# Optimization experiments

Hardware: AMD Instinct MI355X
Metric: run time of the kernel (lower is better)

The kernel has to match this reference:

```python
import jax, jax.numpy as jnp
import numpy as np

EPS = 1e-5

def layer_norm(x, g, b):
    mu = jnp.mean(x, axis=-1, keepdims=True)
    var = jnp.var(x, axis=-1, keepdims=True)
    return (x - mu) * jax.lax.rsqrt(var + EPS) * g + b

def mlp2_ln(x, w1, b1, g, bt, w2, b2):
    # 2-layer NN: Linear -> LayerNorm -> GELU -> Linear
    h = jax.nn.gelu(layer_norm(x @ w1 + b1, g, bt))
    return h @ w2 + b2

def mlp2(x, w1, b1, w2, b2):
    # 2-layer NN without norm: Linear -> GELU -> Linear
    return jax.nn.gelu(x @ w1 + b1) @ w2 + b2

def setup_inputs() -> dict:
    key = jax.random.key(0)
    ks = jax.random.split(key, 20)
    BS, N, D, M, SG = 64, 10000, 128, 16, 1000
    s = lambda i, shp: jax.random.normal(ks[i], shp, dtype=jnp.float32) * (1.0 / np.sqrt(shp[0]))
    return {
        "node_emb": jax.random.normal(ks[0], (BS, N, D), dtype=jnp.float32),
        "graph_emb": jax.random.normal(ks[1], (BS, D), dtype=jnp.float32),
        "sg_node_idx": jax.random.randint(ks[2], (BS, SG), 0, N),
        "sg_meta_features": jax.random.normal(ks[3], (BS, M), dtype=jnp.float32),
        # sg_net: in 2*D -> D -> D
        "sg_w1": s(4, (2 * D, D)), "sg_b1": jnp.zeros((D,), jnp.float32),
        "sg_g": jnp.ones((D,), jnp.float32), "sg_bt": jnp.zeros((D,), jnp.float32),
        "sg_w2": s(5, (D, D)), "sg_b2": jnp.zeros((D,), jnp.float32),
        # meta_feat_net: M -> D -> D
        "mf_w1": s(6, (M, D)), "mf_b1": jnp.zeros((D,), jnp.float32),
        "mf_g": jnp.ones((D,), jnp.float32), "mf_bt": jnp.zeros((D,), jnp.float32),
        "mf_w2": s(7, (D, D)), "mf_b2": jnp.zeros((D,), jnp.float32),
        # ctxt_net: 2*D -> D -> D, no norm
        "cx_w1": s(8, (2 * D, D)), "cx_b1": jnp.zeros((D,), jnp.float32),
        "cx_w2": s(9, (D, D)), "cx_b2": jnp.zeros((D,), jnp.float32),
    }

def reference(node_emb, graph_emb, sg_node_idx, sg_meta_features,
              sg_w1, sg_b1, sg_g, sg_bt, sg_w2, sg_b2,
              mf_w1, mf_b1, mf_g, mf_bt, mf_w2, mf_b2,
              cx_w1, cx_b1, cx_w2, cx_b2):
    # node_emb[:, 0] = 0  (depot / padding sentinel)
    node_emb = node_emb.at[:, 0].set(0.0)
    # gather (BS, sg_n_max, D)
    gathered = jnp.take_along_axis(node_emb, sg_node_idx[:, :, None], axis=1)
    # pooling: sum then max over subgraph nodes, concatenated -> (BS, 2*D)
    pooled = jnp.concatenate([gathered.sum(axis=1), gathered.max(axis=1)], axis=-1)
    sg_emb = (mlp2_ln(pooled, sg_w1, sg_b1, sg_g, sg_bt, sg_w2, sg_b2)
              + mlp2_ln(sg_meta_features, mf_w1, mf_b1, mf_g, mf_bt, mf_w2, mf_b2))
    ctxt_emb = mlp2(jnp.concatenate([sg_emb, graph_emb], axis=-1), cx_w1, cx_b1, cx_w2, cx_b2)
    return sg_emb, ctxt_emb
```

## Files before the change

### kernel.cpp

```cpp
#include <hip/hip_runtime.h>
#include <math.h>

#define BS    64
#define NPTS  10000
#define D     128
#define MM    16
#define SG    1000
#define ROWG  32
#define QS    8

__device__ __forceinline__ float gelu_f(float x) {
    float x3 = x * x * x;
    return 0.5f * x * (1.0f + tanhf(0.7978845608028654f * (x + 0.044715f * x3)));
}

__device__ __forceinline__ float block_sum_q0(float h, int t, int q, int d, float* red) {
    __syncthreads();
    if (q == 0) red[d] = h;
    __syncthreads();
    if (t < 64) {
        float v = red[t] + red[t + 64];
        #pragma unroll
        for (int off = 32; off; off >>= 1) v += __shfl_xor(v, off, 64);
        if (t == 0) red[0] = v;
    }
    __syncthreads();
    return red[0];
}

__global__ __launch_bounds__(1024) void fused_kernel(
    const float* __restrict__ node_emb, const int* __restrict__ sg_idx,
    const float* __restrict__ graph_emb, const float* __restrict__ meta,
    const float* __restrict__ sg_w1, const float* __restrict__ sg_b1,
    const float* __restrict__ sg_g,  const float* __restrict__ sg_bt,
    const float* __restrict__ sg_w2, const float* __restrict__ sg_b2,
    const float* __restrict__ mf_w1, const float* __restrict__ mf_b1,
    const float* __restrict__ mf_g,  const float* __restrict__ mf_bt,
    const float* __restrict__ mf_w2, const float* __restrict__ mf_b2,
    const float* __restrict__ cx_w1, const float* __restrict__ cx_b1,
    const float* __restrict__ cx_w2, const float* __restrict__ cx_b2,
    float* __restrict__ out)
{
    const int b = blockIdx.x;
    const int t = threadIdx.x;

    __shared__ int   idx_lds[SG];
    __shared__ float ssum[ROWG][D];
    __shared__ float smax[ROWG][D];
    __shared__ float xbuf[2 * D];
    __shared__ float part[QS][D];
    __shared__ float hbuf[D];
    __shared__ float osum[D];
    __shared__ float red[D];

    if (t < SG) idx_lds[t] = sg_idx[b * SG + t];
    __syncthreads();

    {
        const int g = t >> 5;
        const int c = t & 31;
        const float* __restrict__ base = node_emb + (size_t)b * NPTS * D;

        float4 s = make_float4(0.f, 0.f, 0.f, 0.f);
        float4 m = make_float4(-INFINITY, -INFINITY, -INFINITY, -INFINITY);

        #pragma unroll 8
        for (int j = g; j < SG; j += ROWG) {
            int id = idx_lds[j];
            float4 v = *(const float4*)(base + (size_t)id * D + (c << 2));
            float msk = (id != 0) ? 1.f : 0.f;
            v.x *= msk; v.y *= msk; v.z *= msk; v.w *= msk;
            s.x += v.x; s.y += v.y; s.z += v.z; s.w += v.w;
            m.x = fmaxf(m.x, v.x); m.y = fmaxf(m.y, v.y);
            m.z = fmaxf(m.z, v.z); m.w = fmaxf(m.w, v.w);
        }
        *(float4*)&ssum[g][c * 4] = s;
        *(float4*)&smax[g][c * 4] = m;
    }
    __syncthreads();

    const int q = t >> 7;
    const int d = t & 127;

    {
        float rs = ssum[q * 4 + 0][d] + ssum[q * 4 + 1][d]
                 + ssum[q * 4 + 2][d] + ssum[q * 4 + 3][d];
        float rm = fmaxf(fmaxf(smax[q * 4 + 0][d], smax[q * 4 + 1][d]),
                         fmaxf(smax[q * 4 + 2][d], smax[q * 4 + 3][d]));
        __syncthreads();
        ssum[q][d] = rs;
        smax[q][d] = rm;
        __syncthreads();
        if (q == 0) {
            float fs = 0.f;
            #pragma unroll
            for (int r = 0; r < QS; ++r) fs += ssum[r][d];
            xbuf[d] = fs;
        } else if (q == 1) {
            float fm = -INFINITY;
            #pragma unroll
            for (int r = 0; r < QS; ++r) fm = fmaxf(fm, smax[r][d]);
            xbuf[D + d] = fm;
        }
        __syncthreads();
    }

    {
        float acc = 0.f;
        const int k0 = q * 32;
        #pragma unroll 8
        for (int kk = 0; kk < 32; ++kk)
            acc = fmaf(xbuf[k0 + kk], sg_w1[(k0 + kk) * D + d], acc);
        part[q][d] = acc;
        __syncthreads();
    }
    {
        float h = 0.f;
        if (q == 0) {
            #pragma unroll
            for (int r = 0; r < QS; ++r) h += part[r][d];
            h += sg_b1[d];
        }
        float mu  = block_sum_q0(h, t, q, d, red) * (1.f / D);
        float cd  = (q == 0) ? (h - mu) : 0.f;
        float var = block_sum_q0(cd * cd, t, q, d, red) * (1.f / D);
        if (q == 0) hbuf[d] = gelu_f(cd * rsqrtf(var + 1e-5f) * sg_g[d] + sg_bt[d]);
        __syncthreads();
    }

    {
        float acc = 0.f;
        const int k0 = q * 16;
        #pragma unroll 8
        for (int kk = 0; kk < 16; ++kk)
            acc = fmaf(hbuf[k0 + kk], sg_w2[(k0 + kk) * D + d], acc);
        part[q][d] = acc;
        __syncthreads();
        if (q == 0) {
            float o = sg_b2[d];
            #pragma unroll
            for (int r = 0; r < QS; ++r) o += part[r][d];
            osum[d] = o;
        }
        __syncthreads();
    }

    {
        float acc = 0.f;
        const int k0 = q * 2;
        #pragma unroll
        for (int kk = 0; kk < 2; ++kk)
            acc = fmaf(meta[b * MM + k0 + kk], mf_w1[(k0 + kk) * D + d], acc);
        part[q][d] = acc;
        __syncthreads();
    }
    {
        float h = 0.f;
        if (q == 0) {
            #pragma unroll
            for (int r = 0; r < QS; ++r) h += part[r][d];
            h += mf_b1[d];
        }
        float mu  = block_sum_q0(h, t, q, d, red) * (1.f / D);
        float cd  = (q == 0) ? (h - mu) : 0.f;
        float var = block_sum_q0(cd * cd, t, q, d, red) * (1.f / D);
        if (q == 0) hbuf[d] = gelu_f(cd * rsqrtf(var + 1e-5f) * mf_g[d] + mf_bt[d]);
        __syncthreads();
    }

    {
        float acc = 0.f;
        const int k0 = q * 16;
        #pragma unroll 8
        for (int kk = 0; kk < 16; ++kk)
            acc = fmaf(hbuf[k0 + kk], mf_w2[(k0 + kk) * D + d], acc);
        part[q][d] = acc;
        __syncthreads();
        if (q == 0) {
            float sg = osum[d] + mf_b2[d];
            #pragma unroll
            for (int r = 0; r < QS; ++r) sg += part[r][d];
            out[b * D + d] = sg;
            xbuf[d] = sg;
        } else if (q == 1) {
            xbuf[D + d] = graph_emb[b * D + d];
        }
        __syncthreads();
    }

    {
        float acc = 0.f;
        const int k0 = q * 32;
        #pragma unroll 8
        for (int kk = 0; kk < 32; ++kk)
            acc = fmaf(xbuf[k0 + kk], cx_w1[(k0 + kk) * D + d], acc);
        part[q][d] = acc;
        __syncthreads();
        if (q == 0) {
            float h = cx_b1[d];
            #pragma unroll
            for (int r = 0; r < QS; ++r) h += part[r][d];
            hbuf[d] = gelu_f(h);
        }
        __syncthreads();
    }

    {
        float acc = 0.f;
        const int k0 = q * 16;
        #pragma unroll 8
        for (int kk = 0; kk < 16; ++kk)
            acc = fmaf(hbuf[k0 + kk], cx_w2[(k0 + kk) * D + d], acc);
        part[q][d] = acc;
        __syncthreads();
        if (q == 0) {
            float o = cx_b2[d];
            #pragma unroll
            for (int r = 0; r < QS; ++r) o += part[r][d];
            out[BS * D + b * D + d] = o;
        }
    }
}

extern "C" void kernel_launch(void* const* d_in, const int* in_sizes, int n_in,
                              void* d_out, int out_size, void* d_ws, size_t ws_size,
                              hipStream_t stream) {
    const float* node_emb  = (const float*)d_in[0];
    const float* graph_emb = (const float*)d_in[1];
    const int*   sg_idx    = (const int*)d_in[2];
    const float* meta      = (const float*)d_in[3];
    const float* sg_w1 = (const float*)d_in[4];
    const float* sg_b1 = (const float*)d_in[5];
    const float* sg_g  = (const float*)d_in[6];
    const float* sg_bt = (const float*)d_in[7];
    const float* sg_w2 = (const float*)d_in[8];
    const float* sg_b2 = (const float*)d_in[9];
    const float* mf_w1 = (const float*)d_in[10];
    const float* mf_b1 = (const float*)d_in[11];
    const float* mf_g  = (const float*)d_in[12];
    const float* mf_bt = (const float*)d_in[13];
    const float* mf_w2 = (const float*)d_in[14];
    const float* mf_b2 = (const float*)d_in[15];
    const float* cx_w1 = (const float*)d_in[16];
    const float* cx_b1 = (const float*)d_in[17];
    const float* cx_w2 = (const float*)d_in[18];
    const float* cx_b2 = (const float*)d_in[19];

    float* out = (float*)d_out;

    fused_kernel<<<BS, 1024, 0, stream>>>(node_emb, sg_idx, graph_emb, meta,
        sg_w1, sg_b1, sg_g, sg_bt, sg_w2, sg_b2,
        mf_w1, mf_b1, mf_g, mf_bt, mf_w2, mf_b2,
        cx_w1, cx_b1, cx_w2, cx_b2, out);
}
```

Before: 23.49 us.

## Split gather across four blocks per batch with atomic counter handoff

The kernel now launches four blocks per batch row, each pooling a quarter of the subgraph indices. Non-leader blocks write partial sums and maxes to workspace and bump an atomic counter, and the leader spin-waits before merging and running the MLPs. The sg and mf first layers and their LayerNorms are also computed together with single-pass mean/variance statistics, cutting barriers. This spreads the memory-bound gather over more CUs. In exchange it adds a memset launch, a spin-wait that assumes all blocks are co-resident, and a one-pass variance formula that is less numerically stable.

Measured after the change: 30.86 us. +31.3%, slower.

```diff
diff --git a/kernel.cpp b/kernel.cpp
--- a/kernel.cpp
+++ b/kernel.cpp
@@ -6,6 +6,8 @@
 #define D     128
 #define MM    16
 #define SG    1000
+#define NPART 4
+#define ROWS  (SG / NPART)
 #define ROWG  32
 #define QS    8
 
@@ -14,18 +16,11 @@
     return 0.5f * x * (1.0f + tanhf(0.7978845608028654f * (x + 0.044715f * x3)));
 }
 
-__device__ __forceinline__ float block_sum_q0(float h, int t, int q, int d, float* red) {
-    __syncthreads();
-    if (q == 0) red[d] = h;
-    __syncthreads();
-    if (t < 64) {
-        float v = red[t] + red[t + 64];
-        #pragma unroll
-        for (int off = 32; off; off >>= 1) v += __shfl_xor(v, off, 64);
-        if (t == 0) red[0] = v;
-    }
-    __syncthreads();
-    return red[0];
+__device__ __forceinline__ void st_dev(float* p, float v) {
+    __hip_atomic_store(p, v, __ATOMIC_RELAXED, __HIP_MEMORY_SCOPE_AGENT);
+}
+__device__ __forceinline__ float ld_dev(const float* p) {
+    return __hip_atomic_load(p, __ATOMIC_RELAXED, __HIP_MEMORY_SCOPE_AGENT);
 }
 
 __global__ __launch_bounds__(1024) void fused_kernel(
@@ -39,21 +34,26 @@
     const float* __restrict__ mf_w2, const float* __restrict__ mf_b2,
     const float* __restrict__ cx_w1, const float* __restrict__ cx_b1,
     const float* __restrict__ cx_w2, const float* __restrict__ cx_b2,
+    int* __restrict__ cnt,
+    float* __restrict__ ws_sum,
+    float* __restrict__ ws_max,
     float* __restrict__ out)
 {
-    const int b = blockIdx.x;
-    const int t = threadIdx.x;
-
-    __shared__ int   idx_lds[SG];
+    const int b    = blockIdx.x & (BS - 1);
+    const int part = blockIdx.x >> 6;
+    const int t    = threadIdx.x;
+
+    __shared__ int   idx_lds[256];
     __shared__ float ssum[ROWG][D];
     __shared__ float smax[ROWG][D];
     __shared__ float xbuf[2 * D];
-    __shared__ float part[QS][D];
-    __shared__ float hbuf[D];
-    __shared__ float osum[D];
-    __shared__ float red[D];
-
-    if (t < SG) idx_lds[t] = sg_idx[b * SG + t];
+    __shared__ float pbuf[QS][D];
+    __shared__ float hbufA[D];
+    __shared__ float hbufB[D];
+    __shared__ float red_a[D], red_b[D], red_c[D], red_d[D];
+    __shared__ float stats[4];
+
+    if (t < ROWS) idx_lds[t] = sg_idx[b * SG + part * ROWS + t];
     __syncthreads();
 
     {
@@ -64,8 +64,8 @@
         float4 s = make_float4(0.f, 0.f, 0.f, 0.f);
         float4 m = make_float4(-INFINITY, -INFINITY, -INFINITY, -INFINITY);
 
-        #pragma unroll 8
-        for (int j = g; j < SG; j += ROWG) {
+        #pragma unroll 4
+        for (int j = g; j < ROWS; j += ROWG) {
             int id = idx_lds[j];
             float4 v = *(const float4*)(base + (size_t)id * D + (c << 2));
             float msk = (id != 0) ? 1.f : 0.f;
@@ -95,91 +95,121 @@
             float fs = 0.f;
             #pragma unroll
             for (int r = 0; r < QS; ++r) fs += ssum[r][d];
-            xbuf[d] = fs;
+            if (part == 0) xbuf[d] = fs;
+            else           st_dev(&ws_sum[(b * (NPART - 1) + part - 1) * D + d], fs);
         } else if (q == 1) {
             float fm = -INFINITY;
             #pragma unroll
             for (int r = 0; r < QS; ++r) fm = fmaxf(fm, smax[r][d]);
-            xbuf[D + d] = fm;
-        }
-        __syncthreads();
-    }
-
-    {
-        float acc = 0.f;
-        const int k0 = q * 32;
-        #pragma unroll 8
-        for (int kk = 0; kk < 32; ++kk)
-            acc = fmaf(xbuf[k0 + kk], sg_w1[(k0 + kk) * D + d], acc);
-        part[q][d] = acc;
-        __syncthreads();
-    }
-    {
-        float h = 0.f;
-        if (q == 0) {
-            #pragma unroll
-            for (int r = 0; r < QS; ++r) h += part[r][d];
-            h += sg_b1[d];
-        }
-        float mu  = block_sum_q0(h, t, q, d, red) * (1.f / D);
-        float cd  = (q == 0) ? (h - mu) : 0.f;
-        float var = block_sum_q0(cd * cd, t, q, d, red) * (1.f / D);
-        if (q == 0) hbuf[d] = gelu_f(cd * rsqrtf(var + 1e-5f) * sg_g[d] + sg_bt[d]);
-        __syncthreads();
-    }
-
-    {
-        float acc = 0.f;
-        const int k0 = q * 16;
-        #pragma unroll 8
-        for (int kk = 0; kk < 16; ++kk)
-            acc = fmaf(hbuf[k0 + kk], sg_w2[(k0 + kk) * D + d], acc);
-        part[q][d] = acc;
-        __syncthreads();
-        if (q == 0) {
-            float o = sg_b2[d];
-            #pragma unroll
-            for (int r = 0; r < QS; ++r) o += part[r][d];
-            osum[d] = o;
-        }
-        __syncthreads();
-    }
-
-    {
-        float acc = 0.f;
-        const int k0 = q * 2;
-        #pragma unroll
-        for (int kk = 0; kk < 2; ++kk)
-            acc = fmaf(meta[b * MM + k0 + kk], mf_w1[(k0 + kk) * D + d], acc);
-        part[q][d] = acc;
-        __syncthreads();
-    }
-    {
-        float h = 0.f;
-        if (q == 0) {
-            #pragma unroll
-            for (int r = 0; r < QS; ++r) h += part[r][d];
-            h += mf_b1[d];
-        }
-        float mu  = block_sum_q0(h, t, q, d, red) * (1.f / D);
-        float cd  = (q == 0) ? (h - mu) : 0.f;
-        float var = block_sum_q0(cd * cd, t, q, d, red) * (1.f / D);
-        if (q == 0) hbuf[d] = gelu_f(cd * rsqrtf(var + 1e-5f) * mf_g[d] + mf_bt[d]);
-        __syncthreads();
-    }
-
-    {
-        float acc = 0.f;
-        const int k0 = q * 16;
-        #pragma unroll 8
-        for (int kk = 0; kk < 16; ++kk)
-            acc = fmaf(hbuf[k0 + kk], mf_w2[(k0 + kk) * D + d], acc);
-        part[q][d] = acc;
-        __syncthreads();
-        if (q == 0) {
-            float sg = osum[d] + mf_b2[d];
-            #pragma unroll
-            for (int r = 0; r < QS; ++r) sg += part[r][d];
+            if (part == 0) xbuf[D + d] = fm;
+            else           st_dev(&ws_max[(b * (NPART - 1) + part - 1) * D + d], fm);
+        }
+        __syncthreads();
+    }
+
+    if (part != 0) {
+        if (t == 0)
+            __hip_atomic_fetch_add(&cnt[b], 1, __ATOMIC_RELEASE, __HIP_MEMORY_SCOPE_AGENT);
+        return;
+    }
+
+    if (t == 0) {
+        long guard = 0;
+        while (__hip_atomic_load(&cnt[b], __ATOMIC_ACQUIRE, __HIP_MEMORY_SCOPE_AGENT)
+                   < NPART - 1 && ++guard < 200000000L) {}
+    }
+    __syncthreads();
+
+    if (q == 0) {
+        float fs = xbuf[d];
+        #pragma unroll
+        for (int h = 0; h < NPART - 1; ++h)
+            fs += ld_dev(&ws_sum[(b * (NPART - 1) + h) * D + d]);
+        xbuf[d] = fs;
+    } else if (q == 1) {
+        float fm = xbuf[D + d];
+        #pragma unroll
+        for (int h = 0; h < NPART - 1; ++h)
+            fm = fmaxf(fm, ld_dev(&ws_max[(b * (NPART - 1) + h) * D + d]));
+        xbuf[D + d] = fm;
+    }
+    __syncthreads();
+
+    {
+        float acc = 0.f;
+        if (q < 4) {
+            const int k0 = q * 64;
+            #pragma unroll 8
+            for (int kk = 0; kk < 64; ++kk)
+                acc = fmaf(xbuf[k0 + kk], sg_w1[(k0 + kk) * D + d], acc);
+        } else {
+            const int k0 = (q - 4) * 4;
+            #pragma unroll
+            for (int kk = 0; kk < 4; ++kk)
+                acc = fmaf(meta[b * MM + k0 + kk], mf_w1[(k0 + kk) * D + d], acc);
+        }
+        pbuf[q][d] = acc;
+        __syncthreads();
+    }
+
+    float h_sg = 0.f, h_mf = 0.f;
+    if (q == 0) {
+        h_sg = pbuf[0][d] + pbuf[1][d] + pbuf[2][d] + pbuf[3][d] + sg_b1[d];
+        red_a[d] = h_sg; red_b[d] = h_sg * h_sg;
+    } else if (q == 1) {
+        h_mf = pbuf[4][d] + pbuf[5][d] + pbuf[6][d] + pbuf[7][d] + mf_b1[d];
+        red_c[d] = h_mf; red_d[d] = h_mf * h_mf;
+    }
+    __syncthreads();
+    if (t < 64) {
+        float v1 = red_a[t] + red_a[t + 64];
+        float v2 = red_b[t] + red_b[t + 64];
+        #pragma unroll
+        for (int off = 32; off; off >>= 1) {
+            v1 += __shfl_xor(v1, off, 64);
+            v2 += __shfl_xor(v2, off, 64);
+        }
+        if (t == 0) { stats[0] = v1 * (1.f / D); stats[1] = v2 * (1.f / D); }
+    } else if (t < 128) {
+        const int l = t - 64;
+        float v1 = red_c[l] + red_c[l + 64];
+        float v2 = red_d[l] + red_d[l + 64];
+        #pragma unroll
+        for (int off = 32; off; off >>= 1) {
+            v1 += __shfl_xor(v1, off, 64);
+            v2 += __shfl_xor(v2, off, 64);
+        }
+        if (l == 0) { stats[2] = v1 * (1.f / D); stats[3] = v2 * (1.f / D); }
+    }
+    __syncthreads();
+    if (q == 0) {
+        float mu = stats[0], var = stats[1] - mu * mu;
+        hbufA[d] = gelu_f((h_sg - mu) * rsqrtf(var + 1e-5f) * sg_g[d] + sg_bt[d]);
+    } else if (q == 1) {
+        float mu = stats[2], var = stats[3] - mu * mu;
+        hbufB[d] = gelu_f((h_mf - mu) * rsqrtf(var + 1e-5f) * mf_g[d] + mf_bt[d]);
+    }
+    __syncthreads();
+
+    {
+        float acc = 0.f;
+        if (q < 4) {
+            const int k0 = q * 32;
+            #pragma unroll 8
+            for (int kk = 0; kk < 32; ++kk)
+                acc = fmaf(hbufA[k0 + kk], sg_w2[(k0 + kk) * D + d], acc);
+        } else {
+            const int k0 = (q - 4) * 32;
+            #pragma unroll 8
+            for (int kk = 0; kk < 32; ++kk)
+                acc = fmaf(hbufB[k0 + kk], mf_w2[(k0 + kk) * D + d], acc);
+        }
+        pbuf[q][d] = acc;
+        __syncthreads();
+        if (q == 0) {
+            float sg = sg_b2[d] + mf_b2[d];
+            #pragma unroll
+            for (int r = 0; r < QS; ++r) sg += pbuf[r][d];
             out[b * D + d] = sg;
             xbuf[d] = sg;
         } else if (q == 1) {
@@ -194,13 +224,13 @@
         #pragma unroll 8
         for (int kk = 0; kk < 32; ++kk)
             acc = fmaf(xbuf[k0 + kk], cx_w1[(k0 + kk) * D + d], acc);
-        part[q][d] = acc;
+        pbuf[q][d] = acc;
         __syncthreads();
         if (q == 0) {
             float h = cx_b1[d];
             #pragma unroll
-            for (int r = 0; r < QS; ++r) h += part[r][d];
-            hbuf[d] = gelu_f(h);
+            for (int r = 0; r < QS; ++r) h += pbuf[r][d];
+            hbufA[d] = gelu_f(h);
         }
         __syncthreads();
     }
@@ -210,13 +240,13 @@
         const int k0 = q * 16;
         #pragma unroll 8
         for (int kk = 0; kk < 16; ++kk)
-            acc = fmaf(hbuf[k0 + kk], cx_w2[(k0 + kk) * D + d], acc);
-        part[q][d] = acc;
+            acc = fmaf(hbufA[k0 + kk], cx_w2[(k0 + kk) * D + d], acc);
+        pbuf[q][d] = acc;
         __syncthreads();
         if (q == 0) {
             float o = cx_b2[d];
             #pragma unroll
-            for (int r = 0; r < QS; ++r) o += part[r][d];
+            for (int r = 0; r < QS; ++r) o += pbuf[r][d];
             out[BS * D + b * D + d] = o;
         }
     }
@@ -247,9 +277,13 @@
     const float* cx_b2 = (const float*)d_in[19];
 
     float* out = (float*)d_out;
-
-    fused_kernel<<<BS, 1024, 0, stream>>>(node_emb, sg_idx, graph_emb, meta,
+    int*   cnt    = (int*)d_ws;
+    float* ws_sum = (float*)((char*)d_ws + 1024);
+    float* ws_max = ws_sum + BS * (NPART - 1) * D;
+
+    hipMemsetAsync(d_ws, 0, 256, stream);
+    fused_kernel<<<BS * NPART, 1024, 0, stream>>>(node_emb, sg_idx, graph_emb, meta,
         sg_w1, sg_b1, sg_g, sg_bt, sg_w2, sg_b2,
         mf_w1, mf_b1, mf_g, mf_bt, mf_w2, mf_b2,
-        cx_w1, cx_b1, cx_w2, cx_b2, out);
-}
+        cx_w1, cx_b1, cx_w2, cx_b2, cnt, ws_sum, ws_max, out);
+}
```
